# Performance work log

Hardware: AMD Instinct MI355X
Metric: run time of the kernel (lower is better)

## Reference

```python
import jax, jax.numpy as jnp
import numpy as np


def setup_inputs() -> dict:
    key = jax.random.key(0)
    ks = jax.random.split(key, 6)
    B, T, U = 4, 160, 80
    De, Dd = 640, 640
    inner, vocab = 640, 1024
    return {
        "enc_state": jax.random.normal(ks[0], (B, T, De), jnp.float32),
        "dec_state": jax.random.normal(ks[1], (B, U, Dd), jnp.float32),
        "W1": jax.random.normal(ks[2], (De + Dd, inner), jnp.float32) * (1.0 / np.sqrt(De + Dd)),
        "b1": jax.random.normal(ks[3], (inner,), jnp.float32) * 0.02,
        "W2": jax.random.normal(ks[4], (inner, vocab), jnp.float32) * (1.0 / np.sqrt(inner)),
        "b2": jax.random.normal(ks[5], (vocab,), jnp.float32) * 0.02,
    }


def reference(enc_state, dec_state, W1, b1, W2, b2):
    # Faithful to: cat([enc tiled over U, dec tiled over T], -1) @ W1 + b1,
    # algebraically split so the [B,T,U,2D] concat is never materialized:
    # cat(e, d) @ W1 == e @ W1[:De] + d @ W1[De:]
    De = enc_state.shape[-1]
    W1_enc, W1_dec = W1[:De], W1[De:]
    enc_proj = jnp.einsum("btd,dh->bth", enc_state, W1_enc)   # [B,T,H]
    dec_proj = jnp.einsum("bud,dh->buh", dec_state, W1_dec)   # [B,U,H]
    # broadcast add over the (T,U) lattice -> [B,T,U,H]
    hidden = jnp.tanh(enc_proj[:, :, None, :] + dec_proj[:, None, :, :] + b1)
    logits = jnp.einsum("btuh,hv->btuv", hidden, W2) + b2     # [B,T,U,V]
    return logits
```

## Files before the change

kernel.cpp:

```cpp
#include <hip/hip_runtime.h>
#include <hip/hip_bf16.h>
#include <cstdint>

#define D_    640
#define V_    1024
#define M_    51200

typedef __bf16 bf16x8 __attribute__((ext_vector_type(8)));
typedef float floatx4 __attribute__((ext_vector_type(4)));

__device__ __forceinline__ void g2l16(const void* g, void* l) {
    __builtin_amdgcn_global_load_lds((const __attribute__((address_space(1))) void*)g,
                                     (__attribute__((address_space(3))) void*)l,
                                     16, 0, 0);
}

__device__ __forceinline__ float fast_tanh(float x) {
    float e = __builtin_amdgcn_exp2f(x * 2.8853900817779268f);
    return 1.0f - 2.0f * __builtin_amdgcn_rcpf(e + 1.0f);
}

__global__ __launch_bounds__(256) void proj_kernel(
    const float* __restrict__ enc, const float* __restrict__ dec,
    const float* __restrict__ W1, const float* __restrict__ b1,
    float* __restrict__ encp, float* __restrict__ decp) {
    __shared__ float As[64][36];
    __shared__ float Ws[32][68];

    const int rt = blockIdx.y;
    const int ct = blockIdx.x;
    const bool is_enc = (rt < 10);
    const float* Asrc; const float* Wsrc; float* Cdst;
    if (is_enc) { Asrc = enc + (size_t)rt * 64 * D_;        Wsrc = W1;           Cdst = encp + (size_t)rt * 64 * D_; }
    else        { Asrc = dec + (size_t)(rt - 10) * 64 * D_; Wsrc = W1 + D_ * D_; Cdst = decp + (size_t)(rt - 10) * 64 * D_; }

    const int tid = threadIdx.x;
    const int ar = tid >> 2,  ac = (tid & 3) * 8;
    const int wr2 = tid >> 3, wc2 = (tid & 7) * 8;
    const int tr = tid >> 4,  tc = tid & 15;

    float acc[4][4] = {};
    for (int k0 = 0; k0 < D_; k0 += 32) {
        __syncthreads();
        *(floatx4*)&As[ar][ac]       = *(const floatx4*)&Asrc[(size_t)ar * D_ + k0 + ac];
        *(floatx4*)&As[ar][ac + 4]   = *(const floatx4*)&Asrc[(size_t)ar * D_ + k0 + ac + 4];
        *(floatx4*)&Ws[wr2][wc2]     = *(const floatx4*)&Wsrc[(size_t)(k0 + wr2) * D_ + ct * 64 + wc2];
        *(floatx4*)&Ws[wr2][wc2 + 4] = *(const floatx4*)&Wsrc[(size_t)(k0 + wr2) * D_ + ct * 64 + wc2 + 4];
        __syncthreads();
#pragma unroll
        for (int kk = 0; kk < 32; kk++) {
            floatx4 w = *(const floatx4*)&Ws[kk][tc * 4];
            float a0 = As[tr * 4 + 0][kk], a1 = As[tr * 4 + 1][kk];
            float a2 = As[tr * 4 + 2][kk], a3 = As[tr * 4 + 3][kk];
#pragma unroll
            for (int j = 0; j < 4; j++) {
                acc[0][j] += a0 * w[j]; acc[1][j] += a1 * w[j];
                acc[2][j] += a2 * w[j]; acc[3][j] += a3 * w[j];
            }
        }
    }
    floatx4 bv = {0.f, 0.f, 0.f, 0.f};
    if (is_enc) bv = *(const floatx4*)&b1[ct * 64 + tc * 4];
#pragma unroll
    for (int i = 0; i < 4; i++) {
        floatx4 v = { acc[i][0] + bv[0], acc[i][1] + bv[1],
                      acc[i][2] + bv[2], acc[i][3] + bv[3] };
        *(floatx4*)&Cdst[(size_t)(tr * 4 + i) * D_ + ct * 64 + tc * 4] = v;
    }
}

__global__ __launch_bounds__(256) void w2t_kernel(
    const float* __restrict__ W2, __bf16* __restrict__ W2t) {
    __shared__ __bf16 tile[32][33];
    const int vt = blockIdx.x;
    const int kt = blockIdx.y;
    const int tx = threadIdx.x & 31, ty = threadIdx.x >> 5;
#pragma unroll
    for (int i = 0; i < 4; i++)
        tile[ty + i * 8][tx] = (__bf16)W2[(size_t)(kt * 32 + ty + i * 8) * V_ + vt * 32 + tx];
    __syncthreads();
#pragma unroll
    for (int i = 0; i < 4; i++)
        W2t[(size_t)(vt * 32 + ty + i * 8) * D_ + kt * 32 + tx] = tile[tx][ty + i * 8];
}

#define SCB  __builtin_amdgcn_sched_barrier(0)

__global__ __launch_bounds__(256, 2) void joint_kernel(
    const float* __restrict__ encp, const float* __restrict__ decp,
    const __bf16* __restrict__ W2t, const float* __restrict__ b2,
    float* __restrict__ C) {
    __shared__ __align__(128) char lds[81920];

    const int bid = blockIdx.x;
    const int swz = (bid & 7) * 400 + (bid >> 3);
    const int mt = swz >> 2, nt = swz & 3;
    const int m0 = mt * 64, n0 = nt * 256;

    const int tid = threadIdx.x;
    const int w = tid >> 6, l = tid & 63;
    const int lr = l & 15, lk = l >> 4;

    char* ldsp = (char*)lds;

    const char* Wb = (const char*)W2t
        + (size_t)(n0 + (tid >> 3)) * 1280
        + (unsigned)((((tid & 7) ^ ((tid >> 3) & 7)) * 16));
    const unsigned bdst = 16384u + (unsigned)tid * 16u;

    const int pr = tid >> 2;
    const int kq = tid & 3;
    const int R  = m0 + pr;
    const int bt = R / 80;
    const int uu = R - bt * 80;
    const int drw = (bt / 160) * 80 + uu;
    const float* ep = encp + (size_t)bt * D_ + kq * 16;
    const float* dp = decp + (size_t)drw * D_ + kq * 16;
    const unsigned pw0 = (unsigned)(pr * 128 + (((kq * 2)     ^ (pr & 7)) * 16));
    const unsigned pw1 = (unsigned)(pr * 128 + (((kq * 2 + 1) ^ (pr & 7)) * 16));

    floatx4 acc[4][4] = {};

#define STAGE_B(BUF, T) do { \
    const char* _s = Wb + (size_t)(T) * 128; \
    char* _d = ldsp + bdst + (BUF) * 32768; \
    g2l16(_s,           _d); \
    g2l16(_s +  40960,  _d +  4096); \
    g2l16(_s +  81920,  _d +  8192); \
    g2l16(_s + 122880,  _d + 12288); \
    g2l16(_s + 163840,  _d + 16384); \
    g2l16(_s + 204800,  _d + 20480); \
    g2l16(_s + 245760,  _d + 24576); \
    g2l16(_s + 286720,  _d + 28672); \
  } while (0)

#define LOAD_ED2(T, EV, DV) do { \
    const float* _e = ep + (T) * 64; const float* _d = dp + (T) * 64; \
    _Pragma("unroll") for (int q = 0; q < 4; ++q) { \
      EV[q] = *(const floatx4*)(_e + q * 4); \
      DV[q] = *(const floatx4*)(_d + q * 4); \
    } } while (0)

#define PRODUCE_A2(BUF, EV, DV) do { \
    bf16x8 h0, h1; \
    _Pragma("unroll") for (int q = 0; q < 4; ++q) { \
      _Pragma("unroll") for (int i2 = 0; i2 < 4; ++i2) { \
        float t_ = fast_tanh(EV[q][i2] + DV[q][i2]); \
        if (q < 2) h0[q * 4 + i2] = (__bf16)t_; else h1[(q - 2) * 4 + i2] = (__bf16)t_; \
      } } \
    *(bf16x8*)(ldsp + (BUF) * 8192 + pw0) = h0; \
    *(bf16x8*)(ldsp + (BUF) * 8192 + pw1) = h1; \
  } while (0)

#define FRAGS_MFMA(BUF) do { \
    _Pragma("unroll") \
    for (int s = 0; s < 2; ++s) { \
        const unsigned sx = (unsigned)((((s * 4 + lk) ^ (lr & 7)) * 16)); \
        bf16x8 af[4], bfr[4]; \
        _Pragma("unroll") for (int i = 0; i < 4; ++i) \
            af[i] = *(const bf16x8*)(ldsp + (BUF) * 8192 + (i * 16 + lr) * 128 + sx); \
        _Pragma("unroll") for (int j = 0; j < 4; ++j) \
            bfr[j] = *(const bf16x8*)(ldsp + 16384 + (BUF) * 32768 + (w * 64 + j * 16 + lr) * 128 + sx); \
        _Pragma("unroll") for (int i = 0; i < 4; ++i) \
            _Pragma("unroll") for (int j = 0; j < 4; ++j) \
                acc[i][j] = __builtin_amdgcn_mfma_f32_16x16x32_bf16(af[i], bfr[j], acc[i][j], 0, 0, 0); \
    } } while (0)

    floatx4 eC[4] = {}, dC[4] = {}, eN[4] = {}, dN[4] = {};

    STAGE_B(0, 0);
    SCB;
    {
        floatx4 e0[4], d0[4];
        LOAD_ED2(0, e0, d0);
        LOAD_ED2(1, eC, dC);
        PRODUCE_A2(0, e0, d0);
    }
    SCB;
    asm volatile("s_waitcnt vmcnt(8) lgkmcnt(0)" ::: "memory");
    __builtin_amdgcn_s_barrier();
    SCB;

#pragma unroll 1
    for (int t = 0; t < 9; ++t) {
        const int buf = t & 1, nb = buf ^ 1;
        STAGE_B(nb, t + 1);
        SCB;
        if (t < 8) LOAD_ED2(t + 2, eN, dN);
        FRAGS_MFMA(buf);
        PRODUCE_A2(nb, eC, dC);
#pragma unroll
        for (int q = 0; q < 4; ++q) { eC[q] = eN[q]; dC[q] = dN[q]; }
        SCB;
        if (t == 8) { asm volatile("s_waitcnt vmcnt(0) lgkmcnt(0)" ::: "memory"); }
        else        { asm volatile("s_waitcnt vmcnt(8) lgkmcnt(0)" ::: "memory"); }
        __builtin_amdgcn_s_barrier();
        SCB;
    }
    FRAGS_MFMA(1);

#pragma unroll
    for (int j = 0; j < 4; ++j) {
        const int col = n0 + w * 64 + j * 16 + lr;
        const float bj = b2[col];
#pragma unroll
        for (int i = 0; i < 4; ++i) {
            const int row = m0 + i * 16 + lk * 4;
            float* Cp = C + (size_t)row * V_ + col;
#pragma unroll
            for (int rg = 0; rg < 4; ++rg)
                Cp[(size_t)rg * V_] = acc[i][j][rg] + bj;
        }
    }
#undef STAGE_B
#undef LOAD_ED2
#undef PRODUCE_A2
#undef FRAGS_MFMA
}

extern "C" void kernel_launch(void* const* d_in, const int* in_sizes, int n_in,
                              void* d_out, int out_size, void* d_ws, size_t ws_size,
                              hipStream_t stream) {
    const float* enc = (const float*)d_in[0];
    const float* dec = (const float*)d_in[1];
    const float* W1  = (const float*)d_in[2];
    const float* b1  = (const float*)d_in[3];
    const float* W2  = (const float*)d_in[4];
    const float* b2  = (const float*)d_in[5];
    float* out = (float*)d_out;

    char* ws = (char*)d_ws;
    float*  encp = (float*)ws;
    float*  decp = (float*)(ws + 1638400);
    __bf16* W2t  = (__bf16*)(ws + 1638400 + 819200);

    proj_kernel<<<dim3(10, 15), 256, 0, stream>>>(enc, dec, W1, b1, encp, decp);
    w2t_kernel<<<dim3(32, 20), 256, 0, stream>>>(W2, W2t);
    joint_kernel<<<3200, 256, 0, stream>>>(encp, decp, W2t, b2, out);
}
```

Baseline: 331.4 us.

## Double joint kernel M tile to 128 rows and simplify the pipeline

The joint GEMM block tile grows from 64x256 to 128x256, so each loaded W2t tile is reused across twice as many rows and the grid drops to 1600 blocks. Each thread now builds the tanh activation tile for half a row with a single A buffer. The hand-scheduled pipeline is removed: the prefetched enc/dec registers, sched barriers and explicit waitcnt control are replaced by plain __syncthreads around MFMA, B staging and A production. This cuts W2t traffic per output and simplifies the code. In exchange, global loads and tanh work no longer overlap with the MFMAs, and the accumulator register footprint doubles.

```diff
diff --git a/kernel.cpp b/kernel.cpp
--- a/kernel.cpp
+++ b/kernel.cpp
@@ -84,8 +84,6 @@
         W2t[(size_t)(vt * 32 + ty + i * 8) * D_ + kt * 32 + tx] = tile[tx][ty + i * 8];
 }
 
-#define SCB  __builtin_amdgcn_sched_barrier(0)
-
 __global__ __launch_bounds__(256, 2) void joint_kernel(
     const float* __restrict__ encp, const float* __restrict__ decp,
     const __bf16* __restrict__ W2t, const float* __restrict__ b2,
@@ -93,9 +91,9 @@
     __shared__ __align__(128) char lds[81920];
 
     const int bid = blockIdx.x;
-    const int swz = (bid & 7) * 400 + (bid >> 3);
+    const int swz = (bid & 7) * 200 + (bid >> 3);
     const int mt = swz >> 2, nt = swz & 3;
-    const int m0 = mt * 64, n0 = nt * 256;
+    const int m0 = mt * 128, n0 = nt * 256;
 
     const int tid = threadIdx.x;
     const int w = tid >> 6, l = tid & 63;
@@ -108,18 +106,19 @@
         + (unsigned)((((tid & 7) ^ ((tid >> 3) & 7)) * 16));
     const unsigned bdst = 16384u + (unsigned)tid * 16u;
 
-    const int pr = tid >> 2;
-    const int kq = tid & 3;
+    const int pr = tid >> 1;
+    const int kh = (tid & 1) * 32;
     const int R  = m0 + pr;
     const int bt = R / 80;
     const int uu = R - bt * 80;
     const int drw = (bt / 160) * 80 + uu;
-    const float* ep = encp + (size_t)bt * D_ + kq * 16;
-    const float* dp = decp + (size_t)drw * D_ + kq * 16;
-    const unsigned pw0 = (unsigned)(pr * 128 + (((kq * 2)     ^ (pr & 7)) * 16));
-    const unsigned pw1 = (unsigned)(pr * 128 + (((kq * 2 + 1) ^ (pr & 7)) * 16));
-
-    floatx4 acc[4][4] = {};
+    const float* ep = encp + (size_t)bt * D_ + kh;
+    const float* dp = decp + (size_t)drw * D_ + kh;
+    const unsigned prb = (unsigned)(pr * 128);
+    const unsigned ps0 = (unsigned)((tid & 1) * 4);
+    const unsigned px  = (unsigned)(pr & 7);
+
+    floatx4 acc[8][4] = {};
 
 #define STAGE_B(BUF, T) do { \
     const char* _s = Wb + (size_t)(T) * 128; \
@@ -134,68 +133,51 @@
     g2l16(_s + 286720,  _d + 28672); \
   } while (0)
 
-#define LOAD_ED2(T, EV, DV) do { \
-    const float* _e = ep + (T) * 64; const float* _d = dp + (T) * 64; \
-    _Pragma("unroll") for (int q = 0; q < 4; ++q) { \
-      EV[q] = *(const floatx4*)(_e + q * 4); \
-      DV[q] = *(const floatx4*)(_d + q * 4); \
+#define PRODUCE_A(T) do { \
+    _Pragma("unroll") for (int sub = 0; sub < 2; ++sub) { \
+      const float* _e = ep + (T) * 64 + sub * 16; \
+      const float* _d = dp + (T) * 64 + sub * 16; \
+      floatx4 ev[4], dv[4]; \
+      _Pragma("unroll") for (int q = 0; q < 4; ++q) { \
+        ev[q] = *(const floatx4*)(_e + q * 4); \
+        dv[q] = *(const floatx4*)(_d + q * 4); \
+      } \
+      bf16x8 h0, h1; \
+      _Pragma("unroll") for (int q = 0; q < 4; ++q) { \
+        _Pragma("unroll") for (int i2 = 0; i2 < 4; ++i2) { \
+          float t_ = fast_tanh(ev[q][i2] + dv[q][i2]); \
+          if (q < 2) h0[q * 4 + i2] = (__bf16)t_; else h1[(q - 2) * 4 + i2] = (__bf16)t_; \
+        } } \
+      *(bf16x8*)(ldsp + prb + (((ps0 + sub * 2)     ^ px) * 16)) = h0; \
+      *(bf16x8*)(ldsp + prb + (((ps0 + sub * 2 + 1) ^ px) * 16)) = h1; \
     } } while (0)
-
-#define PRODUCE_A2(BUF, EV, DV) do { \
-    bf16x8 h0, h1; \
-    _Pragma("unroll") for (int q = 0; q < 4; ++q) { \
-      _Pragma("unroll") for (int i2 = 0; i2 < 4; ++i2) { \
-        float t_ = fast_tanh(EV[q][i2] + DV[q][i2]); \
-        if (q < 2) h0[q * 4 + i2] = (__bf16)t_; else h1[(q - 2) * 4 + i2] = (__bf16)t_; \
-      } } \
-    *(bf16x8*)(ldsp + (BUF) * 8192 + pw0) = h0; \
-    *(bf16x8*)(ldsp + (BUF) * 8192 + pw1) = h1; \
-  } while (0)
 
 #define FRAGS_MFMA(BUF) do { \
     _Pragma("unroll") \
     for (int s = 0; s < 2; ++s) { \
         const unsigned sx = (unsigned)((((s * 4 + lk) ^ (lr & 7)) * 16)); \
-        bf16x8 af[4], bfr[4]; \
-        _Pragma("unroll") for (int i = 0; i < 4; ++i) \
-            af[i] = *(const bf16x8*)(ldsp + (BUF) * 8192 + (i * 16 + lr) * 128 + sx); \
+        bf16x8 af[8], bfr[4]; \
+        _Pragma("unroll") for (int i = 0; i < 8; ++i) \
+            af[i] = *(const bf16x8*)(ldsp + (i * 16 + lr) * 128 + sx); \
         _Pragma("unroll") for (int j = 0; j < 4; ++j) \
             bfr[j] = *(const bf16x8*)(ldsp + 16384 + (BUF) * 32768 + (w * 64 + j * 16 + lr) * 128 + sx); \
-        _Pragma("unroll") for (int i = 0; i < 4; ++i) \
+        _Pragma("unroll") for (int i = 0; i < 8; ++i) \
             _Pragma("unroll") for (int j = 0; j < 4; ++j) \
                 acc[i][j] = __builtin_amdgcn_mfma_f32_16x16x32_bf16(af[i], bfr[j], acc[i][j], 0, 0, 0); \
     } } while (0)
 
-    floatx4 eC[4] = {}, dC[4] = {}, eN[4] = {}, dN[4] = {};
-
     STAGE_B(0, 0);
-    SCB;
-    {
-        floatx4 e0[4], d0[4];
-        LOAD_ED2(0, e0, d0);
-        LOAD_ED2(1, eC, dC);
-        PRODUCE_A2(0, e0, d0);
-    }
-    SCB;
-    asm volatile("s_waitcnt vmcnt(8) lgkmcnt(0)" ::: "memory");
-    __builtin_amdgcn_s_barrier();
-    SCB;
+    PRODUCE_A(0);
+    __syncthreads();
 
 #pragma unroll 1
     for (int t = 0; t < 9; ++t) {
         const int buf = t & 1, nb = buf ^ 1;
+        FRAGS_MFMA(buf);
+        __syncthreads();
         STAGE_B(nb, t + 1);
-        SCB;
-        if (t < 8) LOAD_ED2(t + 2, eN, dN);
-        FRAGS_MFMA(buf);
-        PRODUCE_A2(nb, eC, dC);
-#pragma unroll
-        for (int q = 0; q < 4; ++q) { eC[q] = eN[q]; dC[q] = dN[q]; }
-        SCB;
-        if (t == 8) { asm volatile("s_waitcnt vmcnt(0) lgkmcnt(0)" ::: "memory"); }
-        else        { asm volatile("s_waitcnt vmcnt(8) lgkmcnt(0)" ::: "memory"); }
-        __builtin_amdgcn_s_barrier();
-        SCB;
+        PRODUCE_A(t + 1);
+        __syncthreads();
     }
     FRAGS_MFMA(1);
 
@@ -204,7 +186,7 @@
         const int col = n0 + w * 64 + j * 16 + lr;
         const float bj = b2[col];
 #pragma unroll
-        for (int i = 0; i < 4; ++i) {
+        for (int i = 0; i < 8; ++i) {
             const int row = m0 + i * 16 + lk * 4;
             float* Cp = C + (size_t)row * V_ + col;
 #pragma unroll
@@ -213,8 +195,7 @@
         }
     }
 #undef STAGE_B
-#undef LOAD_ED2
-#undef PRODUCE_A2
+#undef PRODUCE_A
 #undef FRAGS_MFMA
 }
 
@@ -236,5 +217,5 @@
 
     proj_kernel<<<dim3(10, 15), 256, 0, stream>>>(enc, dec, W1, b1, encp, decp);
     w2t_kernel<<<dim3(32, 20), 256, 0, stream>>>(W2, W2t);
-    joint_kernel<<<3200, 256, 0, stream>>>(encp, decp, W2t, b2, out);
-}
+    joint_kernel<<<1600, 256, 0, stream>>>(encp, decp, W2t, b2, out);
+}
```

Measured after the change: 369.3 us. +11.4%, slower.
